# Kernel optimization log

Hardware: AMD Instinct MI355X
Metric: run time of the kernel (lower is better)

## Reference

```python
import jax, jax.numpy as jnp
import numpy as np

HEAD = 4
D_MODEL = 32
SUB_HEADS = 4  # MultiHeadedAttention(4, 32)
NEG_INF = -1e9


def linear(x, w, b):
    # torch nn.Linear: y = x @ W.T + b, W is [out, in]
    return x @ w.T + b


def conv1x1(x, w, b):
    # x: [B, C, S, S], w: [O, C] (1x1 conv kernel squeezed), b: [O]
    return jnp.einsum('oc,bcij->boij', w, x) + b[None, :, None, None]


def mha(x, mask, w, b):
    # Annotated-transformer MultiHeadedAttention with masked_fill(mask==0, -1e9).
    # x: [B, S, D], mask: [B, S, S] float, w: [4, D, D], b: [4, D]
    B, S, D = x.shape
    H = SUB_HEADS
    dk = D // H
    def split(t):
        return t.reshape(B, S, H, dk).transpose(0, 2, 1, 3)  # [B,H,S,dk]
    q = split(linear(x, w[0], b[0]))
    k = split(linear(x, w[1], b[1]))
    v = split(linear(x, w[2], b[2]))
    scores = jnp.einsum('bhqd,bhkd->bhqk', q, k) / jnp.sqrt(jnp.float32(dk))
    scores = jnp.where(mask[:, None, :, :] == 0, NEG_INF, scores)
    attn = jax.nn.softmax(scores, axis=-1)
    out = jnp.einsum('bhqk,bhkd->bhqd', attn, v)
    out = out.transpose(0, 2, 1, 3).reshape(B, S, D)
    return linear(out, w[3], b[3])


def setup_inputs() -> dict:
    key = jax.random.key(0)
    ks = jax.random.split(key, 16)
    B, S, D = 4, 2048, D_MODEL
    s = 0.05
    inp = {
        'feature': jax.random.normal(ks[0], (B, S, D), jnp.float32),
        'data_mask': jnp.ones((B, S, S), jnp.float32),
        'q_w': jax.random.normal(ks[1], (D, D), jnp.float32) * s,
        'q_b': jnp.zeros((D,), jnp.float32),
        'k_w': jax.random.normal(ks[2], (D, D), jnp.float32) * s,
        'k_b': jnp.zeros((D,), jnp.float32),
        'f1_w': jax.random.normal(ks[3], (2 * HEAD, HEAD), jnp.float32) * s,
        'f1_b': jnp.zeros((2 * HEAD,), jnp.float32),
        'f2_w': jax.random.normal(ks[4], (HEAD, 2 * HEAD), jnp.float32) * s,
        'f2_b': jnp.zeros((HEAD,), jnp.float32),
        'f3_w': jax.random.normal(ks[5], (1, HEAD), jnp.float32) * s,
        'f3_b': jnp.zeros((1,), jnp.float32),
        'pa_w': jax.random.normal(ks[6], (4, D, D), jnp.float32) * s,
        'pa_b': jnp.zeros((4, D), jnp.float32),
        'na_w': jax.random.normal(ks[7], (4, D, D), jnp.float32) * s,
        'na_b': jnp.zeros((4, D), jnp.float32),
        'vp_w': jax.random.normal(ks[8], (D, D), jnp.float32) * s,
        'vp_b': jnp.zeros((D,), jnp.float32),
        'vn_w': jax.random.normal(ks[9], (D, D), jnp.float32) * s,
        'vn_b': jnp.zeros((D,), jnp.float32),
        'gp_w': jax.random.normal(ks[10], (D, D), jnp.float32) * s,
        'gp_b': jnp.zeros((D,), jnp.float32),
    }
    return inp


def reference(feature, data_mask, q_w, q_b, k_w, k_b, f1_w, f1_b, f2_w, f2_b,
              f3_w, f3_b, pa_w, pa_b, na_w, na_b, vp_w, vp_b, vn_w, vn_b,
              gp_w, gp_b):
    B, S, D = feature.shape
    H = HEAD
    dk = D // H
    # Outer Q/K projection and per-head scores: [B, H, S, S]
    q = linear(feature, q_w, q_b).reshape(B, S, H, dk).transpose(0, 2, 1, 3)
    k = linear(feature, k_w, k_b).reshape(B, S, H, dk).transpose(0, 2, 1, 3)
    scores = jnp.einsum('bhqd,bhkd->bhqk', q, k) / jnp.sqrt(jnp.float32(dk))
    # fusion: 1x1 conv stack head -> 2*head -> head -> 1 (no nonlinearity between)
    fused = conv1x1(conv1x1(conv1x1(scores, f1_w, f1_b), f2_w, f2_b), f3_w, f3_b)
    sig = jax.nn.sigmoid(fused)  # [B, 1, S, S]
    p_mask = jnp.where(sig > 0.5, sig, 0.0)
    n_mask = jnp.where(sig <= 0.5, sig, 0.0)
    # Two masked sub-attentions over feature
    p = mha(feature, p_mask[:, 0] * data_mask, pa_w, pa_b)
    n = mha(feature, n_mask[:, 0] * data_mask, na_w, na_b)
    vp = linear(p, vp_w, vp_b)
    vn = linear(n, vn_w, vn_b)
    # NOTE: original code uses gate_p for BOTH ep and en (faithful to source).
    ep = linear(p, gp_w, gp_b)
    en = linear(n, gp_w, gp_b)
    v = jnp.stack((vp, vn), axis=0)            # [2, B, S, D]
    e = jax.nn.softmax(jnp.stack((ep, en), axis=0), axis=0)
    return jnp.sum(v * e, axis=0)              # [B, S, D]
```

## Files before the change

kernel.cpp:

```cpp
#include <hip/hip_runtime.h>
#include <cstddef>

#define BB 4
#define SS 2048
#define DMOD 32
#define AEL (BB*SS*DMOD)
#define QBF0 16
#define KBF0 (QBF0 + AEL)
#define VF0  (KBF0 + AEL)
#define QSP0 (VF0 + AEL)
#define SPLEN 393216
#define KSP0 (QSP0 + SPLEN)
#define MB0  (KSP0 + SPLEN)
#define MWORDS (BB*32*SS)
#define PART0 (MB0 + 4*MWORDS)
#define PSLOT (36*8192)
#define TINY 1e-30f

typedef __attribute__((ext_vector_type(16))) float f32x16;
typedef __attribute__((ext_vector_type(4)))  short bf16x4;
typedef unsigned short ushortt;
typedef unsigned long long u64;

#if defined(__has_builtin)
#if __has_builtin(__builtin_amdgcn_mfma_f32_32x32x8bf16_1k)
#define HAVE_MFMA328 1
#endif
#if __has_builtin(__builtin_amdgcn_perm)
#define HAVE_PERM 1
#endif
#endif

__device__ __forceinline__ f32x16 mfma328(bf16x4 a, bf16x4 b, f32x16 c) {
#ifdef HAVE_MFMA328
    return __builtin_amdgcn_mfma_f32_32x32x8bf16_1k(a, b, c, 0, 0, 0);
#else
    f32x16 d;
    asm volatile("v_mfma_f32_32x32x8_bf16 %0, %1, %2, %3\n\t"
                 "s_nop 7\n\t"
                 "s_nop 7\n\t"
                 "s_nop 3"
                 : "=&v"(d) : "v"(a), "v"(b), "v"(c));
    return d;
#endif
}

__device__ __forceinline__ float fexp2(float x) {
#if defined(__has_builtin)
#if __has_builtin(__builtin_amdgcn_exp2f)
    return __builtin_amdgcn_exp2f(x);
#else
    return exp2f(x);
#endif
#else
    return exp2f(x);
#endif
}

__device__ __forceinline__ ushortt b1(float a) {
    unsigned u = __float_as_uint(a);
    u += 0x7fffu + ((u >> 16) & 1u);
    return (ushortt)(u >> 16);
}
__device__ __forceinline__ float tof(ushortt h) {
    return __uint_as_float(((unsigned)h) << 16);
}
__device__ __forceinline__ unsigned bfpair(float a, float b) {
    unsigned ua = __float_as_uint(a), ub = __float_as_uint(b);
    ua += 0x7fffu + ((ua >> 16) & 1u);
    ub += 0x7fffu + ((ub >> 16) & 1u);
    return (ua >> 16) | (ub & 0xffff0000u);
}
__device__ __forceinline__ unsigned bfpairT(float a, float b) {
#ifdef HAVE_PERM
    return __builtin_amdgcn_perm(__float_as_uint(b), __float_as_uint(a),
                                 0x07060302u);
#else
    return (__float_as_uint(a) >> 16) | (__float_as_uint(b) & 0xffff0000u);
#endif
}
__device__ __forceinline__ bf16x4 packT(float p0, float p1, float p2, float p3) {
    union { unsigned u[2]; bf16x4 v; } c;
    c.u[0] = bfpairT(p0, p1);
    c.u[1] = bfpairT(p2, p3);
    return c.v;
}

__global__ __launch_bounds__(256) void k1_proj(
    const float* __restrict__ feat,
    const float* __restrict__ qw, const float* __restrict__ qb,
    const float* __restrict__ kw, const float* __restrict__ kb,
    const float* __restrict__ paw, const float* __restrict__ pab,
    const float* __restrict__ naw, const float* __restrict__ nab,
    const float* __restrict__ f1w, const float* __restrict__ f2w,
    const float* __restrict__ f3w,
    float* __restrict__ wsf) {
    __shared__ float fls[64 * 33];
    int tid = threadIdx.x;
    int w = tid >> 6, lane = tid & 63;
    int rt = blockIdx.x;
    int mat = blockIdx.y * 4 + w;

    {
        int fl = tid * 8;
        int rl = fl >> 5, dd = fl & 31;
        const float* src = feat + ((size_t)(rt * 64 + rl)) * DMOD + dd;
        float4 a = *(const float4*)(src);
        float4 b4 = *(const float4*)(src + 4);
        float* dst = fls + rl * 33 + dd;
        dst[0] = a.x; dst[1] = a.y; dst[2] = a.z; dst[3] = a.w;
        dst[4] = b4.x; dst[5] = b4.y; dst[6] = b4.z; dst[7] = b4.w;
    }
    __syncthreads();

    const float* W; const float* Bv; float sc = 1.f;
    switch (mat) {
        case 0: W = qw;        Bv = qb;       break;
        case 1: W = kw;        Bv = kb;       break;
        case 2: W = paw;       Bv = pab;      sc = 0.5101370246954918f; break;
        case 3: W = paw+1024;  Bv = pab+32;   break;
        case 4: W = paw+2048;  Bv = pab+64;   break;
        case 5: W = naw;       Bv = nab;      sc = 0.5101370246954918f; break;
        case 6: W = naw+1024;  Bv = nab+32;   break;
        default:W = naw+2048;  Bv = nab+64;   break;
    }

    int row = rt * 64 + lane;
    const float* fr = fls + lane * 33;
    float acc[32];
    #pragma unroll
    for (int o4 = 0; o4 < 32; o4 += 4) {
        float a0 = Bv[o4], a1 = Bv[o4+1], a2 = Bv[o4+2], a3 = Bv[o4+3];
        #pragma unroll
        for (int d = 0; d < DMOD; d++) {
            float fv = fr[d];
            a0 += fv * W[(o4+0)*DMOD + d];
            a1 += fv * W[(o4+1)*DMOD + d];
            a2 += fv * W[(o4+2)*DMOD + d];
            a3 += fv * W[(o4+3)*DMOD + d];
        }
        acc[o4] = a0; acc[o4+1] = a1; acc[o4+2] = a2; acc[o4+3] = a3;
    }

    if (mat < 2) {
        if (mat == 0) {
            float cc[4];
            #pragma unroll
            for (int h = 0; h < 4; h++) {
                float s = 0.f;
                #pragma unroll
                for (int a = 0; a < 4; a++) {
                    float t = 0.f;
                    #pragma unroll
                    for (int bb = 0; bb < 8; bb++) t += f2w[a*8+bb] * f1w[bb*4+h];
                    s += f3w[a] * t;
                }
                cc[h] = s * 0.35355339059327373f;
            }
            #pragma unroll
            for (int o = 0; o < 32; o++) acc[o] *= cc[o >> 3];
        }
        ushortt* base = (ushortt*)(wsf + (mat == 0 ? QSP0 : KSP0));
        size_t tb = (size_t)(row >> 5) * 3;
        int li2 = row & 31;
        ushortt sp[3][32];
        #pragma unroll
        for (int o = 0; o < 32; o++) {
            float v = acc[o];
            ushortt h0 = b1(v);
            float r1 = v - tof(h0);
            ushortt m0 = b1(r1);
            float r2 = r1 - tof(m0);
            sp[0][o] = h0; sp[1][o] = m0; sp[2][o] = b1(r2);
        }
        #pragma unroll
        for (int t = 0; t < 3; t++) {
            ushortt* tb2 = base + (tb + t) * 1024 + li2 * 4;
            #pragma unroll
            for (int ks = 0; ks < 4; ks++) {
                #pragma unroll
                for (int hi2 = 0; hi2 < 2; hi2++) {
                    int c0 = ks*8 + hi2*4;
                    *(ushort4*)(tb2 + (ks*2 + hi2) * 128) =
                        make_ushort4(sp[t][c0], sp[t][c0+1], sp[t][c0+2], sp[t][c0+3]);
                }
            }
        }
        return;
    }

    #pragma unroll
    for (int o = 0; o < 32; o++) acc[o] *= sc;
    int b = row >> 11, r2i = row & 2047;
    int pn = (mat >= 5);
    int bp = (b << 1) | pn;
    int m3 = mat - (pn ? 5 : 2);
    if (m3 < 2) {
        unsigned pk[16];
        #pragma unroll
        for (int i = 0; i < 16; i++) pk[i] = bfpair(acc[2*i], acc[2*i+1]);
        unsigned* dst = (unsigned*)((ushortt*)(wsf + (m3 == 0 ? QBF0 : KBF0))
                         + (size_t)bp*65536 + (size_t)r2i*32);
        #pragma unroll
        for (int i = 0; i < 4; i++)
            *(uint4*)(dst + 4*i) = make_uint4(pk[4*i], pk[4*i+1], pk[4*i+2], pk[4*i+3]);
    } else {
        ushortt* vf = (ushortt*)(wsf + VF0)
                         + (size_t)bp*65536 + (size_t)(r2i>>2)*128 + (r2i&3);
        #pragma unroll
        for (int o = 0; o < 32; o++)
            vf[(size_t)o*4] = b1(acc[o]);
    }
}

__global__ __launch_bounds__(256) void kA_mask(
    const float* __restrict__ dmask,
    const ushortt* __restrict__ qsp, const ushortt* __restrict__ ksp,
    u64* __restrict__ pmout,
    const float* __restrict__ f1b, const float* __restrict__ f2w,
    const float* __restrict__ f2b, const float* __restrict__ f3w,
    const float* __restrict__ f3b) {
    int tid = threadIdx.x;
    int w = tid >> 6, l = tid & 63, li = l & 31, hi = l >> 5;
    int b = blockIdx.z;
    int it = blockIdx.y * 32;
    int j0 = blockIdx.x * 256 + w * 64;

    float cbv = f3b[0];
    #pragma unroll
    for (int a = 0; a < 4; a++) {
        float t = f2b[a];
        #pragma unroll
        for (int bb = 0; bb < 8; bb++) t += f2w[a*8+bb] * f1b[bb];
        cbv += f3w[a] * t;
    }

    size_t qtb = (size_t)((b*SS + it) >> 5) * 3;
    bf16x4 qa[3][4];
    #pragma unroll
    for (int t = 0; t < 3; t++) {
        const ushortt* qb2 = qsp + (qtb + t) * 1024 + hi * 128 + li * 4;
        #pragma unroll
        for (int ks = 0; ks < 4; ks++)
            qa[t][ks] = *(const bf16x4*)(qb2 + ks * 256);
    }

    const float* dmbase = dmask + (size_t)b*SS*SS;
    u64* pm = pmout + (size_t)b*32*SS;
    u64* nm = pmout + MWORDS + (size_t)b*32*SS;

    f32x16 cin;
    #pragma unroll
    for (int r = 0; r < 16; r++) cin[r] = cbv;

    int j64 = j0 >> 6;
    float dm0[16], dm1[16];
    #pragma unroll
    for (int r = 0; r < 16; r++) {
        int i = it + (r & 3) + 8*(r >> 2) + 4*hi;
        const float* dr = dmbase + (size_t)i*SS + j0 + li;
        dm0[r] = dr[0];
        dm1[r] = dr[32];
    }
    f32x16 St[2];
    #pragma unroll
    for (int t2 = 0; t2 < 2; t2++) {
        int jt = j0 + t2*32;
        size_t ktb = (size_t)((b*SS + jt) >> 5) * 3;
        bf16x4 kb[3][4];
        #pragma unroll
        for (int t = 0; t < 3; t++) {
            const ushortt* kb2 = ksp + (ktb + t) * 1024 + hi * 128 + li * 4;
            #pragma unroll
            for (int ks = 0; ks < 4; ks++)
                kb[t][ks] = *(const bf16x4*)(kb2 + ks * 256);
        }
        f32x16 S = cin;
        #pragma unroll
        for (int ks = 0; ks < 4; ks++) S = mfma328(qa[0][ks], kb[0][ks], S);
        #pragma unroll
        for (int ks = 0; ks < 4; ks++) S = mfma328(qa[0][ks], kb[1][ks], S);
        #pragma unroll
        for (int ks = 0; ks < 4; ks++) S = mfma328(qa[1][ks], kb[0][ks], S);
        #pragma unroll
        for (int ks = 0; ks < 4; ks++) S = mfma328(qa[0][ks], kb[2][ks], S);
        #pragma unroll
        for (int ks = 0; ks < 4; ks++) S = mfma328(qa[2][ks], kb[0][ks], S);
        #pragma unroll
        for (int ks = 0; ks < 4; ks++) S = mfma328(qa[1][ks], kb[1][ks], S);
        St[t2] = S;
    }
    #pragma unroll
    for (int r = 0; r < 16; r++) {
        bool a0 = (dm0[r] != 0.f), a1 = (dm1[r] != 0.f);
        bool s0 = St[0][r] > 0.f, s1 = St[1][r] > 0.f;
        u64 b0p = __ballot(s0 && a0);
        u64 b1p = __ballot(s1 && a1);
        u64 b0n = __ballot(!s0 && a0);
        u64 b1n = __ballot(!s1 && a1);
        u64 pA = (b0p & 0xffffffffull) | (b1p << 32);
        u64 pB = (b0p >> 32) | (b1p & 0xffffffff00000000ull);
        u64 nA = (b0n & 0xffffffffull) | (b1n << 32);
        u64 nB = (b0n >> 32) | (b1n & 0xffffffff00000000ull);
        int iA = it + (r & 3) + 8*(r >> 2);
        if (l == 0) {
            pm[(size_t)j64*SS + iA] = pA;
            nm[(size_t)j64*SS + iA] = nA;
        }
        if (l == 32) {
            pm[(size_t)j64*SS + iA + 4] = pB;
            nm[(size_t)j64*SS + iA + 4] = nB;
        }
    }
}

__global__ __launch_bounds__(256) void kB_attn(
    const ushortt* __restrict__ qbf,
    const ushortt* __restrict__ kbf,
    const ushortt* __restrict__ vff,
    const u64* __restrict__ mall,
    float* __restrict__ part, int CJ, int NCH) {
    int tid = threadIdx.x;
    int w = tid >> 6, l = tid & 63, li = l & 31, hi = l >> 5;
    int jc = blockIdx.x, rg = blockIdx.y, z = blockIdx.z;
    int b = z >> 2, pn = (z >> 1) & 1, hp = z & 1;
    int bp = (b << 1) | pn;
    int h0 = hp * 2;
    int it32 = rg * 128 + w * 32;

    const ushortt* qrow = qbf + (size_t)bp*65536 + (size_t)(it32 + li)*32 + 4*hi;
    bf16x4 qf[2];
    #pragma unroll
    for (int hh = 0; hh < 2; hh++) qf[hh] = *(const bf16x4*)(qrow + (h0+hh)*8);

    const ushortt* kbase = kbf + (size_t)bp*65536 + (size_t)li*32 + 4*hi;
    const ushortt* vbase = vff + (size_t)bp*65536 + (size_t)hi*128;
    const u64* msk = mall + (size_t)pn*MWORDS + (size_t)b*32*SS + (it32 + li);

    bool isl8 = (li == 8);
    bf16x4 ones4;
    {
        union { ushortt s[4]; bf16x4 v; } o;
        o.s[0] = o.s[1] = o.s[2] = o.s[3] = 0x3F80;
        ones4 = o.v;
    }

    f32x16 zero16;
    #pragma unroll
    for (int r = 0; r < 16; r++) zero16[r] = 0.f;
    f32x16 oacc[2];
    #pragma unroll
    for (int hh = 0; hh < 2; hh++)
        #pragma unroll
        for (int r = 0; r < 16; r++) oacc[hh][r] = 0.f;

    int j0 = jc * CJ;
    for (int jw = 0; jw < CJ; jw += 64) {
        u64 mw = msk[(size_t)((j0 + jw) >> 6) * SS];
        #pragma unroll
        for (int half = 0; half < 2; half++) {
            int jt = j0 + jw + half*32;
            unsigned m32 = (unsigned)(mw >> (half*32));
            const ushortt* krow = kbase + (size_t)jt*32;
            const ushortt* vrow = vbase + (size_t)(jt>>2)*128;
            #pragma unroll
            for (int hh = 0; hh < 2; hh++) {
                int h = h0 + hh;
                bf16x4 kf = *(const bf16x4*)(krow + h*8);
                int vcol = ((h*8 + li) & 31) * 4;
                bf16x4 vf0 = *(const bf16x4*)(vrow + 0*256 + vcol);
                bf16x4 vf1 = *(const bf16x4*)(vrow + 1*256 + vcol);
                bf16x4 vf2 = *(const bf16x4*)(vrow + 2*256 + vcol);
                bf16x4 vf3 = *(const bf16x4*)(vrow + 3*256 + vcol);
                if (isl8) { vf0 = ones4; vf1 = ones4; vf2 = ones4; vf3 = ones4; }
                f32x16 sacc = mfma328(kf, qf[hh], zero16);
                float p[16];
                #pragma unroll
                for (int r = 0; r < 16; r++) {
                    int sh = (r & 3) + 8*(r >> 2) + 4*hi;
                    float e = fexp2(sacc[r]);
                    p[r] = ((m32 >> sh) & 1u) ? e : TINY;
                }
                oacc[hh] = mfma328(packT(p[0],  p[1],  p[2],  p[3]),  vf0, oacc[hh]);
                oacc[hh] = mfma328(packT(p[4],  p[5],  p[6],  p[7]),  vf1, oacc[hh]);
                oacc[hh] = mfma328(packT(p[8],  p[9],  p[10], p[11]), vf2, oacc[hh]);
                oacc[hh] = mfma328(packT(p[12], p[13], p[14], p[15]), vf3, oacc[hh]);
            }
        }
    }
    float* base2 = part + (size_t)(pn * NCH + jc) * PSLOT + (size_t)b * SS;
    if (isl8) {
        #pragma unroll
        for (int hh = 0; hh < 2; hh++) {
            int h = h0 + hh;
            #pragma unroll
            for (int r = 0; r < 16; r++) {
                int irow = it32 + (r & 3) + 8*(r >> 2) + 4*hi;
                base2[(size_t)h * 8192 + irow] = oacc[hh][r];
            }
        }
    }
    if (li < 8) {
        #pragma unroll
        for (int hh = 0; hh < 2; hh++) {
            int h = h0 + hh;
            #pragma unroll
            for (int r = 0; r < 16; r++) {
                int irow = it32 + (r & 3) + 8*(r >> 2) + 4*hi;
                base2[(size_t)(4 + h*8 + li) * 8192 + irow] = oacc[hh][r];
            }
        }
    }
}

__global__ __launch_bounds__(256) void k3a_red(float* __restrict__ part, int NCH) {
    int idx = blockIdx.x * 256 + threadIdx.x;
    size_t e = (size_t)idx * 4;
    int pn = (int)(e / PSLOT);
    size_t off = e - (size_t)pn * PSLOT;
    float* base = part + (size_t)pn * NCH * PSLOT + off;
    float4 s = *(const float4*)base;
    for (int c = 1; c < NCH; c++) {
        float4 v = *(const float4*)(base + (size_t)c * PSLOT);
        s.x += v.x; s.y += v.y; s.z += v.z; s.w += v.w;
    }
    *(float4*)base = s;
}

__global__ __launch_bounds__(256) void k3b_fin(
    const float* __restrict__ part, int NCH,
    const float* __restrict__ paw, const float* __restrict__ pab,
    const float* __restrict__ naw, const float* __restrict__ nab,
    const float* __restrict__ vpw, const float* __restrict__ vpb,
    const float* __restrict__ vnw, const float* __restrict__ vnb,
    const float* __restrict__ gpw, const float* __restrict__ gpb,
    float* __restrict__ out) {
    __shared__ float sums[8][72];
    __shared__ float Pl[8][64];
    __shared__ float pnv[8][64];
    int tid = threadIdx.x;
    int r = tid >> 5, o = tid & 31;
    int row = blockIdx.x * 8 + r;
    const float* b0 = part + row;
    const float* b1 = part + (size_t)NCH * PSLOT + row;
    for (int v = o; v < 72; v += 32) {
        int pn = v >= 36;
        int k = v - 36 * pn;
        sums[r][v] = (pn ? b1 : b0)[(size_t)k * 8192];
    }
    __syncthreads();
    Pl[r][o]      = sums[r][4 + o]  / sums[r][o >> 3];
    Pl[r][32 + o] = sums[r][40 + o] / sums[r][36 + (o >> 3)];
    __syncthreads();
    const float* pw3 = paw + 3*1024; const float* pb3 = pab + 3*32;
    const float* nw3 = naw + 3*1024; const float* nb3 = nab + 3*32;
    float pv = pb3[o], nv = nb3[o];
    #pragma unroll
    for (int d = 0; d < 32; d++) {
        pv += Pl[r][d]      * pw3[o*32 + d];
        nv += Pl[r][32 + d] * nw3[o*32 + d];
    }
    pnv[r][o] = pv; pnv[r][32 + o] = nv;
    __syncthreads();
    float vp = vpb[o], vn = vnb[o], ep = gpb[o], en = gpb[o];
    #pragma unroll
    for (int d = 0; d < 32; d++) {
        float pd = pnv[r][d], nd = pnv[r][32 + d];
        vp += pd * vpw[o*32 + d];
        vn += nd * vnw[o*32 + d];
        ep += pd * gpw[o*32 + d];
        en += nd * gpw[o*32 + d];
    }
    float g = 1.0f / (1.0f + __expf(en - ep));
    out[(size_t)row * 32 + o] = vp * g + vn * (1.0f - g);
}

extern "C" void kernel_launch(void* const* d_in, const int* in_sizes, int n_in,
                              void* d_out, int out_size, void* d_ws, size_t ws_size,
                              hipStream_t stream) {
    const float* feat  = (const float*)d_in[0];
    const float* dmask = (const float*)d_in[1];
    const float* qw  = (const float*)d_in[2];  const float* qb  = (const float*)d_in[3];
    const float* kw  = (const float*)d_in[4];  const float* kb  = (const float*)d_in[5];
    const float* f1w = (const float*)d_in[6];  const float* f1b = (const float*)d_in[7];
    const float* f2w = (const float*)d_in[8];  const float* f2b = (const float*)d_in[9];
    const float* f3w = (const float*)d_in[10]; const float* f3b = (const float*)d_in[11];
    const float* paw = (const float*)d_in[12]; const float* pab = (const float*)d_in[13];
    const float* naw = (const float*)d_in[14]; const float* nab = (const float*)d_in[15];
    const float* vpw = (const float*)d_in[16]; const float* vpb = (const float*)d_in[17];
    const float* vnw = (const float*)d_in[18]; const float* vnb = (const float*)d_in[19];
    const float* gpw = (const float*)d_in[20]; const float* gpb = (const float*)d_in[21];
    float* wsf = (float*)d_ws;
    float* out = (float*)d_out;

    size_t avail = ws_size / 4;
    int nch = 1;
    if (avail > (size_t)PART0) {
        size_t per = (size_t)2 * PSLOT;
        size_t m = (avail - PART0) / per;
        nch = (m >= 8) ? 8 : (m >= 4) ? 4 : (m >= 2) ? 2 : 1;
    }
    int cj = SS / nch;
    float* part = wsf + PART0;

    const ushortt* qbfu = (const ushortt*)(wsf + QBF0);
    const ushortt* kbfu = (const ushortt*)(wsf + KBF0);
    const ushortt* vffu = (const ushortt*)(wsf + VF0);
    const ushortt* qspu = (const ushortt*)(wsf + QSP0);
    const ushortt* kspu = (const ushortt*)(wsf + KSP0);

    hipLaunchKernelGGL(k1_proj, dim3(128, 2), dim3(256), 0, stream,
                       feat, qw, qb, kw, kb, paw, pab, naw, nab,
                       f1w, f2w, f3w, wsf);
    hipLaunchKernelGGL(kA_mask, dim3(8, 64, BB), dim3(256), 0, stream,
                       dmask, qspu, kspu, (u64*)(wsf + MB0),
                       f1b, f2w, f2b, f3w, f3b);
    hipLaunchKernelGGL(kB_attn, dim3(nch, 16, BB*4), dim3(256), 0, stream,
                       qbfu, kbfu, vffu,
                       (const u64*)(wsf + MB0), part, cj, nch);
    if (nch > 1)
        hipLaunchKernelGGL(k3a_red, dim3(576), dim3(256), 0, stream, part, nch);
    hipLaunchKernelGGL(k3b_fin, dim3(1024), dim3(256), 0, stream,
                       part, nch, paw, pab, naw, nab, vpw, vpb, vnw, vnb, gpw, gpb,
                       out);
}
```

Before: 105.5 us.

## Fuse positive and negative attention branches into one attention block

Each attention block now processes both the positive and negative masked sub-attentions for the same batch, head pair and row tile, rather than launching separate blocks per branch. Because the two masks are complementary, each score needs only one exp, selected by which mask bit is set, and the result is shared by both accumulators. This halves the exponential work and the grid size. The cost is doubled accumulator and fragment registers per thread, which may lower occupancy.

```diff
diff --git a/kernel.cpp b/kernel.cpp
--- a/kernel.cpp
+++ b/kernel.cpp
@@ -323,19 +323,26 @@
     int tid = threadIdx.x;
     int w = tid >> 6, l = tid & 63, li = l & 31, hi = l >> 5;
     int jc = blockIdx.x, rg = blockIdx.y, z = blockIdx.z;
-    int b = z >> 2, pn = (z >> 1) & 1, hp = z & 1;
-    int bp = (b << 1) | pn;
+    int b = z >> 1, hp = z & 1;
+    int bpP = (b << 1), bpN = bpP | 1;
     int h0 = hp * 2;
     int it32 = rg * 128 + w * 32;
 
-    const ushortt* qrow = qbf + (size_t)bp*65536 + (size_t)(it32 + li)*32 + 4*hi;
-    bf16x4 qf[2];
-    #pragma unroll
-    for (int hh = 0; hh < 2; hh++) qf[hh] = *(const bf16x4*)(qrow + (h0+hh)*8);
-
-    const ushortt* kbase = kbf + (size_t)bp*65536 + (size_t)li*32 + 4*hi;
-    const ushortt* vbase = vff + (size_t)bp*65536 + (size_t)hi*128;
-    const u64* msk = mall + (size_t)pn*MWORDS + (size_t)b*32*SS + (it32 + li);
+    const ushortt* qrowP = qbf + (size_t)bpP*65536 + (size_t)(it32 + li)*32 + 4*hi;
+    const ushortt* qrowN = qbf + (size_t)bpN*65536 + (size_t)(it32 + li)*32 + 4*hi;
+    bf16x4 qfP[2], qfN[2];
+    #pragma unroll
+    for (int hh = 0; hh < 2; hh++) {
+        qfP[hh] = *(const bf16x4*)(qrowP + (h0+hh)*8);
+        qfN[hh] = *(const bf16x4*)(qrowN + (h0+hh)*8);
+    }
+
+    const ushortt* kbaseP = kbf + (size_t)bpP*65536 + (size_t)li*32 + 4*hi;
+    const ushortt* kbaseN = kbf + (size_t)bpN*65536 + (size_t)li*32 + 4*hi;
+    const ushortt* vbaseP = vff + (size_t)bpP*65536 + (size_t)hi*128;
+    const ushortt* vbaseN = vff + (size_t)bpN*65536 + (size_t)hi*128;
+    const u64* mskP = mall + (size_t)b*32*SS + (it32 + li);
+    const u64* mskN = mall + (size_t)MWORDS + (size_t)b*32*SS + (it32 + li);
 
     bool isl8 = (li == 8);
     bf16x4 ones4;
@@ -348,47 +355,69 @@
     f32x16 zero16;
     #pragma unroll
     for (int r = 0; r < 16; r++) zero16[r] = 0.f;
-    f32x16 oacc[2];
+    f32x16 oaccP[2], oaccN[2];
     #pragma unroll
     for (int hh = 0; hh < 2; hh++)
         #pragma unroll
-        for (int r = 0; r < 16; r++) oacc[hh][r] = 0.f;
+        for (int r = 0; r < 16; r++) { oaccP[hh][r] = 0.f; oaccN[hh][r] = 0.f; }
 
     int j0 = jc * CJ;
     for (int jw = 0; jw < CJ; jw += 64) {
-        u64 mw = msk[(size_t)((j0 + jw) >> 6) * SS];
+        u64 mwP = mskP[(size_t)((j0 + jw) >> 6) * SS];
+        u64 mwN = mskN[(size_t)((j0 + jw) >> 6) * SS];
         #pragma unroll
         for (int half = 0; half < 2; half++) {
             int jt = j0 + jw + half*32;
-            unsigned m32 = (unsigned)(mw >> (half*32));
-            const ushortt* krow = kbase + (size_t)jt*32;
-            const ushortt* vrow = vbase + (size_t)(jt>>2)*128;
+            unsigned m32p = (unsigned)(mwP >> (half*32));
+            unsigned m32n = (unsigned)(mwN >> (half*32));
+            const ushortt* krowP = kbaseP + (size_t)jt*32;
+            const ushortt* krowN = kbaseN + (size_t)jt*32;
+            const ushortt* vrowP = vbaseP + (size_t)(jt>>2)*128;
+            const ushortt* vrowN = vbaseN + (size_t)(jt>>2)*128;
             #pragma unroll
             for (int hh = 0; hh < 2; hh++) {
                 int h = h0 + hh;
-                bf16x4 kf = *(const bf16x4*)(krow + h*8);
+                bf16x4 kfP = *(const bf16x4*)(krowP + h*8);
+                bf16x4 kfN = *(const bf16x4*)(krowN + h*8);
                 int vcol = ((h*8 + li) & 31) * 4;
-                bf16x4 vf0 = *(const bf16x4*)(vrow + 0*256 + vcol);
-                bf16x4 vf1 = *(const bf16x4*)(vrow + 1*256 + vcol);
-                bf16x4 vf2 = *(const bf16x4*)(vrow + 2*256 + vcol);
-                bf16x4 vf3 = *(const bf16x4*)(vrow + 3*256 + vcol);
-                if (isl8) { vf0 = ones4; vf1 = ones4; vf2 = ones4; vf3 = ones4; }
-                f32x16 sacc = mfma328(kf, qf[hh], zero16);
-                float p[16];
+                bf16x4 vfP0 = *(const bf16x4*)(vrowP + 0*256 + vcol);
+                bf16x4 vfP1 = *(const bf16x4*)(vrowP + 1*256 + vcol);
+                bf16x4 vfP2 = *(const bf16x4*)(vrowP + 2*256 + vcol);
+                bf16x4 vfP3 = *(const bf16x4*)(vrowP + 3*256 + vcol);
+                bf16x4 vfN0 = *(const bf16x4*)(vrowN + 0*256 + vcol);
+                bf16x4 vfN1 = *(const bf16x4*)(vrowN + 1*256 + vcol);
+                bf16x4 vfN2 = *(const bf16x4*)(vrowN + 2*256 + vcol);
+                bf16x4 vfN3 = *(const bf16x4*)(vrowN + 3*256 + vcol);
+                if (isl8) {
+                    vfP0 = ones4; vfP1 = ones4; vfP2 = ones4; vfP3 = ones4;
+                    vfN0 = ones4; vfN1 = ones4; vfN2 = ones4; vfN3 = ones4;
+                }
+                f32x16 saccP = mfma328(kfP, qfP[hh], zero16);
+                f32x16 saccN = mfma328(kfN, qfN[hh], zero16);
+                float p[16], n[16];
                 #pragma unroll
                 for (int r = 0; r < 16; r++) {
                     int sh = (r & 3) + 8*(r >> 2) + 4*hi;
-                    float e = fexp2(sacc[r]);
-                    p[r] = ((m32 >> sh) & 1u) ? e : TINY;
+                    bool bp_ = ((m32p >> sh) & 1u) != 0u;
+                    bool bn_ = ((m32n >> sh) & 1u) != 0u;
+                    float route = bp_ ? saccP[r] : saccN[r];
+                    float e = fexp2(route);
+                    p[r] = bp_ ? e : TINY;
+                    n[r] = bn_ ? e : TINY;
                 }
-                oacc[hh] = mfma328(packT(p[0],  p[1],  p[2],  p[3]),  vf0, oacc[hh]);
-                oacc[hh] = mfma328(packT(p[4],  p[5],  p[6],  p[7]),  vf1, oacc[hh]);
-                oacc[hh] = mfma328(packT(p[8],  p[9],  p[10], p[11]), vf2, oacc[hh]);
-                oacc[hh] = mfma328(packT(p[12], p[13], p[14], p[15]), vf3, oacc[hh]);
+                oaccP[hh] = mfma328(packT(p[0],  p[1],  p[2],  p[3]),  vfP0, oaccP[hh]);
+                oaccP[hh] = mfma328(packT(p[4],  p[5],  p[6],  p[7]),  vfP1, oaccP[hh]);
+                oaccP[hh] = mfma328(packT(p[8],  p[9],  p[10], p[11]), vfP2, oaccP[hh]);
+                oaccP[hh] = mfma328(packT(p[12], p[13], p[14], p[15]), vfP3, oaccP[hh]);
+                oaccN[hh] = mfma328(packT(n[0],  n[1],  n[2],  n[3]),  vfN0, oaccN[hh]);
+                oaccN[hh] = mfma328(packT(n[4],  n[5],  n[6],  n[7]),  vfN1, oaccN[hh]);
+                oaccN[hh] = mfma328(packT(n[8],  n[9],  n[10], n[11]), vfN2, oaccN[hh]);
+                oaccN[hh] = mfma328(packT(n[12], n[13], n[14], n[15]), vfN3, oaccN[hh]);
             }
         }
     }
-    float* base2 = part + (size_t)(pn * NCH + jc) * PSLOT + (size_t)b * SS;
+    float* baseP = part + (size_t)(0 * NCH + jc) * PSLOT + (size_t)b * SS;
+    float* baseN = part + (size_t)(1 * NCH + jc) * PSLOT + (size_t)b * SS;
     if (isl8) {
         #pragma unroll
         for (int hh = 0; hh < 2; hh++) {
@@ -396,7 +425,8 @@
             #pragma unroll
             for (int r = 0; r < 16; r++) {
                 int irow = it32 + (r & 3) + 8*(r >> 2) + 4*hi;
-                base2[(size_t)h * 8192 + irow] = oacc[hh][r];
+                baseP[(size_t)h * 8192 + irow] = oaccP[hh][r];
+                baseN[(size_t)h * 8192 + irow] = oaccN[hh][r];
             }
         }
     }
@@ -407,7 +437,8 @@
             #pragma unroll
             for (int r = 0; r < 16; r++) {
                 int irow = it32 + (r & 3) + 8*(r >> 2) + 4*hi;
-                base2[(size_t)(4 + h*8 + li) * 8192 + irow] = oacc[hh][r];
+                baseP[(size_t)(4 + h*8 + li) * 8192 + irow] = oaccP[hh][r];
+                baseN[(size_t)(4 + h*8 + li) * 8192 + irow] = oaccN[hh][r];
             }
         }
     }
@@ -515,7 +546,7 @@
     hipLaunchKernelGGL(kA_mask, dim3(8, 64, BB), dim3(256), 0, stream,
                        dmask, qspu, kspu, (u64*)(wsf + MB0),
                        f1b, f2w, f2b, f3w, f3b);
-    hipLaunchKernelGGL(kB_attn, dim3(nch, 16, BB*4), dim3(256), 0, stream,
+    hipLaunchKernelGGL(kB_attn, dim3(nch, 16, BB*2), dim3(256), 0, stream,
                        qbfu, kbfu, vffu,
                        (const u64*)(wsf + MB0), part, cj, nch);
     if (nch > 1)
```

New measurement: 107.3 us. About the same (+1.7%).
